# Performance work log

Hardware: AMD Instinct MI355X
Metric: run time of the kernel (lower is better)

Reference implementation:

```python
import jax, jax.numpy as jnp
import numpy as np

EMB = 768
HEADS = 8
HEAD_DIM = EMB // HEADS  # 96


def setup_inputs() -> dict:
    key = jax.random.key(0)
    ks = jax.random.split(key, 9)
    B, S = 16, 1024
    s = 1.0 / np.sqrt(EMB)
    inp = {
        "input_embeddings": jax.random.normal(ks[0], (B, S, EMB), dtype=jnp.float32),
        "Wq": jax.random.normal(ks[1], (EMB, EMB), dtype=jnp.float32) * s,
        "bq": jnp.zeros((EMB,), dtype=jnp.float32),
        "Wk": jax.random.normal(ks[2], (EMB, EMB), dtype=jnp.float32) * s,
        "bk": jnp.zeros((EMB,), dtype=jnp.float32),
        "Wv": jax.random.normal(ks[3], (EMB, EMB), dtype=jnp.float32) * s,
        "bv": jnp.zeros((EMB,), dtype=jnp.float32),
        "Wo": jax.random.normal(ks[4], (EMB, EMB), dtype=jnp.float32) * s,
        "bo": jnp.zeros((EMB,), dtype=jnp.float32),
    }
    return inp


def reference(input_embeddings, Wq, bq, Wk, bk, Wv, bv, Wo, bo):
    B, S, _ = input_embeddings.shape
    # QKV projections (torch Linear: x @ W.T + b; here W stored as [in,out])
    q = input_embeddings @ Wq + bq
    k = input_embeddings @ Wk + bk
    v = input_embeddings @ Wv + bv
    # [B, H, S, Dh]
    q = q.reshape(B, S, HEADS, HEAD_DIM).transpose(0, 2, 1, 3)
    k = k.reshape(B, S, HEADS, HEAD_DIM).transpose(0, 2, 1, 3)
    v = v.reshape(B, S, HEADS, HEAD_DIM).transpose(0, 2, 1, 3)
    scores = jnp.einsum("bhqd,bhkd->bhqk", q, k) / np.sqrt(HEAD_DIM)
    probs = jax.nn.softmax(scores, axis=-1)  # dropout=0 (eval)
    context = jnp.einsum("bhqk,bhkd->bhqd", probs, v)
    context = context.transpose(0, 2, 1, 3).reshape(B, S, HEADS * HEAD_DIM)
    output = context @ Wo + bo
    return (output, probs)
```

## Files before the change

kernel.cpp:

```cpp
#include <hip/hip_runtime.h>

typedef _Float16 half8 __attribute__((ext_vector_type(8)));
typedef _Float16 half4 __attribute__((ext_vector_type(4)));
typedef float f32x4 __attribute__((ext_vector_type(4)));

__device__ __forceinline__ void lds_load16(const void* g, void* l) {
  __builtin_amdgcn_global_load_lds((const __attribute__((address_space(1))) void*)g,
                                   (__attribute__((address_space(3))) void*)l, 16, 0, 0);
}

__global__ __launch_bounds__(256) void cvt_all(const float* __restrict__ X,
                                               const float* __restrict__ Wq, const float* __restrict__ Wk,
                                               const float* __restrict__ Wv, const float* __restrict__ Wo,
                                               _Float16* __restrict__ Xh,
                                               _Float16* __restrict__ Wqkvt, _Float16* __restrict__ Wot) {
  const int bid = blockIdx.x, tid = threadIdx.x;
  if (bid < 6144) {
    int i = bid * 256 + tid;
    const float4* p = (const float4*)(X + (size_t)i * 8);
    float4 a = p[0], b = p[1];
    half8 v;
    v[0] = (_Float16)a.x; v[1] = (_Float16)a.y; v[2] = (_Float16)a.z; v[3] = (_Float16)a.w;
    v[4] = (_Float16)b.x; v[5] = (_Float16)b.y; v[6] = (_Float16)b.z; v[7] = (_Float16)b.w;
    *(half8*)(Xh + (size_t)i * 8) = v;
  } else {
    int id = (bid - 6144) * 256 + tid;
    int part = id / 589824;
    int r = id - part * 589824;
    int k = r / 768;
    int n = r - k * 768;
    const float* W = part == 0 ? Wq : part == 1 ? Wk : part == 2 ? Wv : Wo;
    _Float16 v = (_Float16)W[(size_t)k * 768 + n];
    if (part < 3) Wqkvt[((size_t)(part * 768 + n)) * 768 + k] = v;
    else          Wot[(size_t)n * 768 + k] = v;
  }
}

template <int EPI, int NB>
__global__ __launch_bounds__(256, 4) void gemm128(
    const _Float16* __restrict__ A, const _Float16* __restrict__ Bt,
    const float* __restrict__ b0, const float* __restrict__ b1, const float* __restrict__ b2,
    _Float16* __restrict__ Qo, _Float16* __restrict__ Ko, _Float16* __restrict__ Vto,
    float* __restrict__ Co) {
  __shared__ _Float16 Ab[2][128 * 32];
  __shared__ _Float16 Bb[2][128 * 32];
  const int tid = threadIdx.x, w = tid >> 6, l = tid & 63;
  const int lr = l & 15, lk = l >> 4;
  const int wm = w >> 1, wn = w & 1;
  const int q8 = (int)gridDim.x >> 3;
  const int wg = ((int)blockIdx.x & 7) * q8 + ((int)blockIdx.x >> 3);
  const int m0 = (wg / NB) * 128, n0 = (wg % NB) * 128;

  auto STAGE = [&](int kt, int dstb) {
#pragma unroll
    for (int i = 0; i < 2; ++i) {
      const int g = i * 256 + tid;
      const int row = g >> 2;
      const int gr = (g & 3) ^ (row & 3);
      lds_load16(A + (size_t)(m0 + row) * 768 + kt * 32 + gr * 8,
                 (char*)&Ab[dstb][0] + g * 16);
      lds_load16(Bt + (size_t)(n0 + row) * 768 + kt * 32 + gr * 8,
                 (char*)&Bb[dstb][0] + g * 16);
    }
  };

  f32x4 acc[4][4] = {};
  STAGE(0, 0);
  const int swzg = ((lk ^ (lr & 3)) * 8);

  for (int T = 0; T < 24; ++T) {
    const int b = T & 1;
    asm volatile("s_waitcnt vmcnt(0)" ::: "memory");
    asm volatile("s_barrier" ::: "memory");
    if (T < 23) STAGE(T + 1, b ^ 1);
    half8 af[4], bf[4];
#pragma unroll
    for (int mi = 0; mi < 4; ++mi)
      af[mi] = *(const half8*)&Ab[b][(wm * 64 + mi * 16 + lr) * 32 + swzg];
#pragma unroll
    for (int ni = 0; ni < 4; ++ni)
      bf[ni] = *(const half8*)&Bb[b][(wn * 64 + ni * 16 + lr) * 32 + swzg];
    __builtin_amdgcn_s_setprio(1);
#pragma unroll
    for (int mi = 0; mi < 4; ++mi)
#pragma unroll
      for (int ni = 0; ni < 4; ++ni)
        acc[mi][ni] = __builtin_amdgcn_mfma_f32_16x16x32_f16(af[mi], bf[ni], acc[mi][ni], 0, 0, 0);
    __builtin_amdgcn_s_setprio(0);
  }

#pragma unroll
  for (int mi = 0; mi < 4; ++mi) {
    const int rbase = m0 + wm * 64 + mi * 16 + lk * 4;
#pragma unroll
    for (int ni = 0; ni < 4; ++ni) {
      const int col = n0 + wn * 64 + ni * 16 + lr;
      if (EPI == 0) {
        const int part = col / 768;
        const int e = col - part * 768;
        const int h = e / 96, d = e - (e / 96) * 96;
        const float* bb = part == 0 ? b0 : part == 1 ? b1 : b2;
        const float bv = bb[e];
#pragma unroll
        for (int j = 0; j < 4; ++j) {
          const int row = rbase + j;
          const int bI = row >> 10, s = row & 1023;
          const int bh = bI * 8 + h;
          const _Float16 v = (_Float16)(acc[mi][ni][j] + bv);
          if (part < 2) {
            const size_t idx = ((((size_t)(bh * 64 + (s >> 4)) * 3 + (d >> 5)) * 64
                                + ((d & 31) >> 3) * 16 + (s & 15)) << 3) + (d & 7);
            if (part == 0) Qo[idx] = v; else Ko[idx] = v;
          } else {
            const size_t idx = ((((size_t)(bh * 6 + (d >> 4)) * 32 + (s >> 5)) * 64
                                + ((s & 31) >> 3) * 16 + (d & 15)) << 3) + (s & 7);
            Vto[idx] = v;
          }
        }
      } else {
        const float bv = b0[col];
#pragma unroll
        for (int j = 0; j < 4; ++j) {
          const int row = rbase + j;
          __builtin_nontemporal_store(acc[mi][ni][j] + bv, Co + (size_t)row * 768 + col);
        }
      }
    }
  }
}

__global__ __launch_bounds__(512, 4) void attn(const _Float16* __restrict__ swzQ,
                                               const _Float16* __restrict__ swzK,
                                               const _Float16* __restrict__ swzV,
                                               float* __restrict__ probs,
                                               _Float16* __restrict__ ctx) {
  __shared__ _Float16 Ps[8][2][16][136];
  __shared__ float lsb[8][2][16];
  const int tid = threadIdx.x, w = tid >> 6, l = tid & 63;
  const int lr = l & 15, lk = l >> 4;
  const int id = blockIdx.x;
  const int lid = (id & 7) * 512 + (id >> 3);
  const int bh = lid >> 5, qt2 = lid & 31;
  const int q0 = qt2 * 32;
  const float SC = 0.10206207261596577f * 1.4426950408889634f;
  const int b = bh >> 3, h = bh & 7;

  const half8* qbA = (const half8*)swzQ + (size_t)(bh * 64 + qt2 * 2) * 192;
  const half8* kb  = (const half8*)swzK + (size_t)(bh * 64 + w * 8) * 192;
  const half8* vb0 = (const half8*)swzV + (size_t)bh * 12288;

  half8 bqA[3], bqB[3];
#pragma unroll
  for (int kk = 0; kk < 3; ++kk) { bqA[kk] = qbA[kk * 64 + l]; bqB[kk] = qbA[192 + kk * 64 + l]; }

  f32x4 sA[8], sB[8];
#pragma unroll
  for (int cb = 0; cb < 4; ++cb) {
    half8 kf[2][3];
#pragma unroll
    for (int t = 0; t < 2; ++t)
#pragma unroll
      for (int kk = 0; kk < 3; ++kk) kf[t][kk] = kb[((cb * 2 + t) * 3 + kk) * 64 + l];
#pragma unroll
    for (int t = 0; t < 2; ++t) {
      const int ct = cb * 2 + t;
      f32x4 aA = {0.f, 0.f, 0.f, 0.f}, aB = {0.f, 0.f, 0.f, 0.f};
#pragma unroll
      for (int kk = 0; kk < 3; ++kk) {
        aA = __builtin_amdgcn_mfma_f32_16x16x32_f16(kf[t][kk], bqA[kk], aA, 0, 0, 0);
        aB = __builtin_amdgcn_mfma_f32_16x16x32_f16(kf[t][kk], bqB[kk], aB, 0, 0, 0);
      }
      sA[ct] = aA; sB[ct] = aB;
    }
  }

  float psA = 0.f, psB = 0.f;
#pragma unroll
  for (int ct = 0; ct < 8; ++ct)
#pragma unroll
    for (int j = 0; j < 4; ++j) {
      const float eA = __builtin_amdgcn_exp2f(sA[ct][j] * SC);
      const float eB = __builtin_amdgcn_exp2f(sB[ct][j] * SC);
      sA[ct][j] = eA; psA += eA;
      sB[ct][j] = eB; psB += eB;
    }
  psA += __shfl_xor(psA, 16); psA += __shfl_xor(psA, 32);
  psB += __shfl_xor(psB, 16); psB += __shfl_xor(psB, 32);
  if (lk == 0) { lsb[w][0][lr] = psA; lsb[w][1][lr] = psB; }
  __syncthreads();
  float ltA = 0.f, ltB = 0.f;
#pragma unroll
  for (int ww = 0; ww < 8; ++ww) { ltA += lsb[ww][0][lr]; ltB += lsb[ww][1][lr]; }
  const float invlA = 1.f / ltA, invlB = 1.f / ltB;

  float* pbA = probs + ((size_t)bh << 20) + (size_t)(q0 + lr) * 1024 + w * 128 + lk * 4;
#pragma unroll
  for (int ct = 0; ct < 8; ++ct) {
    f32x4 pA4, pB4;
    half4 phA, phB;
#pragma unroll
    for (int j = 0; j < 4; ++j) {
      const float pA = sA[ct][j] * invlA;
      const float pB = sB[ct][j] * invlB;
      pA4[j] = pA; phA[j] = (_Float16)pA;
      pB4[j] = pB; phB[j] = (_Float16)pB;
    }
    __builtin_nontemporal_store(pA4, (f32x4*)(pbA + ct * 16));
    __builtin_nontemporal_store(pB4, (f32x4*)(pbA + 16 * 1024 + ct * 16));
    *(half4*)&Ps[w][0][lr][ct * 16 + lk * 4] = phA;
    *(half4*)&Ps[w][1][lr][ct * 16 + lk * 4] = phB;
  }

  f32x4 cA[6] = {}, cB[6] = {};
#pragma unroll
  for (int kk = 0; kk < 4; ++kk) {
    half8 vf[6];
#pragma unroll
    for (int dt = 0; dt < 6; ++dt) vf[dt] = vb0[(dt * 32 + w * 4 + kk) * 64 + l];
    half8 paA = *(const half8*)&Ps[w][0][lr][kk * 32 + lk * 8];
    half8 paB = *(const half8*)&Ps[w][1][lr][kk * 32 + lk * 8];
#pragma unroll
    for (int dt = 0; dt < 6; ++dt) {
      cA[dt] = __builtin_amdgcn_mfma_f32_16x16x32_f16(paA, vf[dt], cA[dt], 0, 0, 0);
      cB[dt] = __builtin_amdgcn_mfma_f32_16x16x32_f16(paB, vf[dt], cB[dt], 0, 0, 0);
    }
  }

  _Float16* cpA = &Ps[w][0][0][0];
  _Float16* cpB = &Ps[w][1][0][0];
#pragma unroll
  for (int dt = 0; dt < 6; ++dt)
#pragma unroll
    for (int j = 0; j < 4; ++j) {
      cpA[(lk * 4 + j) * 100 + dt * 16 + lr] = (_Float16)cA[dt][j];
      cpB[(lk * 4 + j) * 100 + dt * 16 + lr] = (_Float16)cB[dt][j];
    }
  __syncthreads();

  const int rq = tid >> 5;
  const int rd0 = (tid & 31) * 3;
#pragma unroll
  for (int t = 0; t < 2; ++t) {
    _Float16* cg = ctx + ((size_t)(b * 1024 + q0 + t * 16 + rq)) * 768 + h * 96 + rd0;
#pragma unroll
    for (int e = 0; e < 3; ++e) {
      float v = 0.f;
#pragma unroll
      for (int ww = 0; ww < 8; ++ww)
        v += (float)((const _Float16*)&Ps[ww][t][0][0])[rq * 100 + rd0 + e];
      cg[e] = (_Float16)v;
    }
  }
}

extern "C" void kernel_launch(void* const* d_in, const int* in_sizes, int n_in,
                              void* d_out, int out_size, void* d_ws, size_t ws_size,
                              hipStream_t stream) {
  (void)in_sizes; (void)n_in; (void)out_size; (void)ws_size;
  const float* X  = (const float*)d_in[0];
  const float* Wq = (const float*)d_in[1];
  const float* bq = (const float*)d_in[2];
  const float* Wk = (const float*)d_in[3];
  const float* bk = (const float*)d_in[4];
  const float* Wv = (const float*)d_in[5];
  const float* bv = (const float*)d_in[6];
  const float* Wo = (const float*)d_in[7];
  const float* bo = (const float*)d_in[8];

  char* ws = (char*)d_ws;
  _Float16* Xh    = (_Float16*)(ws + 0);
  _Float16* Wqkvt = (_Float16*)(ws + 25165824);
  _Float16* Wot   = (_Float16*)(ws + 28704768);
  _Float16* Qh    = (_Float16*)(ws + 29884416);
  _Float16* Kh    = (_Float16*)(ws + 55050240);
  _Float16* Vth   = (_Float16*)(ws + 80216064);
  _Float16* Ctx   = (_Float16*)(ws + 105381888);

  float* out   = (float*)d_out;
  float* probs = out + 12582912;

  cvt_all<<<dim3(15360), dim3(256), 0, stream>>>(X, Wq, Wk, Wv, Wo, Xh, Wqkvt, Wot);
  gemm128<0, 18><<<dim3(2304), dim3(256), 0, stream>>>(Xh, Wqkvt, bq, bk, bv, Qh, Kh, Vth, nullptr);
  attn<<<dim3(4096), dim3(512), 0, stream>>>(Qh, Kh, Vth, probs, Ctx);
  gemm128<1, 6><<<dim3(768), dim3(256), 0, stream>>>(Ctx, Wot, bo, bo, bo, nullptr, nullptr, nullptr, out);
}
```

Measured before the change: 371.8 us.

## Tile weight transpose through LDS and defer softmax normalization in attention

The weight conversion now transposes 64x64 tiles through shared memory with coalesced float4 reads and half4 writes, replacing the per-element strided scatter, and the grid shrinks to match. In attention, unnormalized exp values are written as fp16 straight into LDS, dropping the 32 f32x4 score registers. Probs are then re-read from LDS, scaled by a per-row inverse, and stored with a coalesced row layout. The P·V result is scaled by the inverse sum afterwards, and some barriers become raw s_waitcnt/s_barrier. This lowers register pressure and uncoalesced traffic, but the stored probs now pass through fp16 before normalization, which costs some precision.

```diff
diff --git a/kernel.cpp b/kernel.cpp
--- a/kernel.cpp
+++ b/kernel.cpp
@@ -7,6 +7,11 @@
 __device__ __forceinline__ void lds_load16(const void* g, void* l) {
   __builtin_amdgcn_global_load_lds((const __attribute__((address_space(1))) void*)g,
                                    (__attribute__((address_space(3))) void*)l, 16, 0, 0);
+}
+
+__device__ __forceinline__ void lds_barrier() {
+  asm volatile("s_waitcnt lgkmcnt(0)" ::: "memory");
+  asm volatile("s_barrier" ::: "memory");
 }
 
 __global__ __launch_bounds__(256) void cvt_all(const float* __restrict__ X,
@@ -24,15 +29,32 @@
     v[4] = (_Float16)b.x; v[5] = (_Float16)b.y; v[6] = (_Float16)b.z; v[7] = (_Float16)b.w;
     *(half8*)(Xh + (size_t)i * 8) = v;
   } else {
-    int id = (bid - 6144) * 256 + tid;
-    int part = id / 589824;
-    int r = id - part * 589824;
-    int k = r / 768;
-    int n = r - k * 768;
+    __shared__ _Float16 T[64][72];
+    const int t = bid - 6144;
+    const int part = t / 144;
+    const int r = t - part * 144;
+    const int k0 = (r / 12) * 64, n0 = (r - (r / 12) * 12) * 64;
     const float* W = part == 0 ? Wq : part == 1 ? Wk : part == 2 ? Wv : Wo;
-    _Float16 v = (_Float16)W[(size_t)k * 768 + n];
-    if (part < 3) Wqkvt[((size_t)(part * 768 + n)) * 768 + k] = v;
-    else          Wot[(size_t)n * 768 + k] = v;
+    const int lr0 = tid >> 4, lc0 = (tid & 15) * 4;
+#pragma unroll
+    for (int rr = 0; rr < 4; ++rr) {
+      const int row = lr0 + rr * 16;
+      float4 v = *(const float4*)(W + (size_t)(k0 + row) * 768 + n0 + lc0);
+      T[lc0 + 0][row] = (_Float16)v.x;
+      T[lc0 + 1][row] = (_Float16)v.y;
+      T[lc0 + 2][row] = (_Float16)v.z;
+      T[lc0 + 3][row] = (_Float16)v.w;
+    }
+    __syncthreads();
+    _Float16* Wt = part < 3 ? (Wqkvt + (size_t)(part * 768 + n0) * 768 + k0)
+                            : (Wot + (size_t)n0 * 768 + k0);
+    const int wr0 = tid >> 4, wc0 = (tid & 15) * 4;
+#pragma unroll
+    for (int rr = 0; rr < 4; ++rr) {
+      const int nrow = wr0 + rr * 16;
+      half4 h = *(const half4*)&T[nrow][wc0];
+      *(half4*)(Wt + (size_t)nrow * 768 + wc0) = h;
+    }
   }
 }
 
@@ -134,8 +156,9 @@
                                                const _Float16* __restrict__ swzV,
                                                float* __restrict__ probs,
                                                _Float16* __restrict__ ctx) {
-  __shared__ _Float16 Ps[8][2][16][136];
+  __shared__ __align__(16) _Float16 Ph[8][2][16][136];
   __shared__ float lsb[8][2][16];
+  __shared__ float invb[2][16];
   const int tid = threadIdx.x, w = tid >> 6, l = tid & 63;
   const int lr = l & 15, lk = l >> 4;
   const int id = blockIdx.x;
@@ -153,14 +176,15 @@
 #pragma unroll
   for (int kk = 0; kk < 3; ++kk) { bqA[kk] = qbA[kk * 64 + l]; bqB[kk] = qbA[192 + kk * 64 + l]; }
 
-  f32x4 sA[8], sB[8];
+  float psA = 0.f, psB = 0.f;
 #pragma unroll
   for (int cb = 0; cb < 4; ++cb) {
     half8 kf[2][3];
 #pragma unroll
     for (int t = 0; t < 2; ++t)
 #pragma unroll
-      for (int kk = 0; kk < 3; ++kk) kf[t][kk] = kb[((cb * 2 + t) * 3 + kk) * 64 + l];
+      for (int kk = 0; kk < 3; ++kk)
+        kf[t][kk] = kb[((cb * 2 + t) * 3 + kk) * 64 + l];
 #pragma unroll
     for (int t = 0; t < 2; ++t) {
       const int ct = cb * 2 + t;
@@ -170,46 +194,54 @@
         aA = __builtin_amdgcn_mfma_f32_16x16x32_f16(kf[t][kk], bqA[kk], aA, 0, 0, 0);
         aB = __builtin_amdgcn_mfma_f32_16x16x32_f16(kf[t][kk], bqB[kk], aB, 0, 0, 0);
       }
-      sA[ct] = aA; sB[ct] = aB;
-    }
-  }
-
-  float psA = 0.f, psB = 0.f;
-#pragma unroll
-  for (int ct = 0; ct < 8; ++ct)
-#pragma unroll
-    for (int j = 0; j < 4; ++j) {
-      const float eA = __builtin_amdgcn_exp2f(sA[ct][j] * SC);
-      const float eB = __builtin_amdgcn_exp2f(sB[ct][j] * SC);
-      sA[ct][j] = eA; psA += eA;
-      sB[ct][j] = eB; psB += eB;
-    }
+      half4 hA, hB;
+#pragma unroll
+      for (int j = 0; j < 4; ++j) {
+        const float eA = __builtin_amdgcn_exp2f(aA[j] * SC);
+        const float eB = __builtin_amdgcn_exp2f(aB[j] * SC);
+        psA += eA; psB += eB;
+        hA[j] = (_Float16)eA; hB[j] = (_Float16)eB;
+      }
+      *(half4*)&Ph[w][0][lr][ct * 16 + lk * 4] = hA;
+      *(half4*)&Ph[w][1][lr][ct * 16 + lk * 4] = hB;
+    }
+  }
   psA += __shfl_xor(psA, 16); psA += __shfl_xor(psA, 32);
   psB += __shfl_xor(psB, 16); psB += __shfl_xor(psB, 32);
   if (lk == 0) { lsb[w][0][lr] = psA; lsb[w][1][lr] = psB; }
-  __syncthreads();
-  float ltA = 0.f, ltB = 0.f;
-#pragma unroll
-  for (int ww = 0; ww < 8; ++ww) { ltA += lsb[ww][0][lr]; ltB += lsb[ww][1][lr]; }
-  const float invlA = 1.f / ltA, invlB = 1.f / ltB;
-
-  float* pbA = probs + ((size_t)bh << 20) + (size_t)(q0 + lr) * 1024 + w * 128 + lk * 4;
-#pragma unroll
-  for (int ct = 0; ct < 8; ++ct) {
-    f32x4 pA4, pB4;
-    half4 phA, phB;
-#pragma unroll
-    for (int j = 0; j < 4; ++j) {
-      const float pA = sA[ct][j] * invlA;
-      const float pB = sB[ct][j] * invlB;
-      pA4[j] = pA; phA[j] = (_Float16)pA;
-      pB4[j] = pB; phB[j] = (_Float16)pB;
-    }
-    __builtin_nontemporal_store(pA4, (f32x4*)(pbA + ct * 16));
-    __builtin_nontemporal_store(pB4, (f32x4*)(pbA + 16 * 1024 + ct * 16));
-    *(half4*)&Ps[w][0][lr][ct * 16 + lk * 4] = phA;
-    *(half4*)&Ps[w][1][lr][ct * 16 + lk * 4] = phB;
-  }
+  lds_barrier();
+  if (tid < 32) {
+    const int t = tid >> 4, q = tid & 15;
+    float lt = 0.f;
+#pragma unroll
+    for (int ww = 0; ww < 8; ++ww) lt += lsb[ww][t][q];
+    invb[t][q] = 1.f / lt;
+  }
+  lds_barrier();
+
+  {
+    const int qh = l >> 5, c4 = (l & 31) * 4;
+#pragma unroll
+    for (int t = 0; t < 2; ++t) {
+      float* pbase = probs + ((size_t)bh << 20) + (size_t)(q0 + t * 16) * 1024 + w * 128;
+#pragma unroll
+      for (int r2 = 0; r2 < 8; ++r2) {
+        const int q = r2 * 2 + qh;
+        half4 hv = *(const half4*)&Ph[w][t][q][c4];
+        const float iv = invb[t][q];
+        f32x4 v;
+#pragma unroll
+        for (int j = 0; j < 4; ++j) v[j] = (float)hv[j] * iv;
+        __builtin_nontemporal_store(v, (f32x4*)(pbase + (size_t)q * 1024 + c4));
+      }
+    }
+  }
+
+  float ivr[2][4];
+#pragma unroll
+  for (int t = 0; t < 2; ++t)
+#pragma unroll
+    for (int j = 0; j < 4; ++j) ivr[t][j] = invb[t][lk * 4 + j];
 
   f32x4 cA[6] = {}, cB[6] = {};
 #pragma unroll
@@ -217,8 +249,8 @@
     half8 vf[6];
 #pragma unroll
     for (int dt = 0; dt < 6; ++dt) vf[dt] = vb0[(dt * 32 + w * 4 + kk) * 64 + l];
-    half8 paA = *(const half8*)&Ps[w][0][lr][kk * 32 + lk * 8];
-    half8 paB = *(const half8*)&Ps[w][1][lr][kk * 32 + lk * 8];
+    half8 paA = *(const half8*)&Ph[w][0][lr][kk * 32 + lk * 8];
+    half8 paB = *(const half8*)&Ph[w][1][lr][kk * 32 + lk * 8];
 #pragma unroll
     for (int dt = 0; dt < 6; ++dt) {
       cA[dt] = __builtin_amdgcn_mfma_f32_16x16x32_f16(paA, vf[dt], cA[dt], 0, 0, 0);
@@ -226,16 +258,16 @@
     }
   }
 
-  _Float16* cpA = &Ps[w][0][0][0];
-  _Float16* cpB = &Ps[w][1][0][0];
+  _Float16* cpA = &Ph[w][0][0][0];
+  _Float16* cpB = &Ph[w][1][0][0];
 #pragma unroll
   for (int dt = 0; dt < 6; ++dt)
 #pragma unroll
     for (int j = 0; j < 4; ++j) {
-      cpA[(lk * 4 + j) * 100 + dt * 16 + lr] = (_Float16)cA[dt][j];
-      cpB[(lk * 4 + j) * 100 + dt * 16 + lr] = (_Float16)cB[dt][j];
-    }
-  __syncthreads();
+      cpA[(lk * 4 + j) * 100 + dt * 16 + lr] = (_Float16)(cA[dt][j] * ivr[0][j]);
+      cpB[(lk * 4 + j) * 100 + dt * 16 + lr] = (_Float16)(cB[dt][j] * ivr[1][j]);
+    }
+  lds_barrier();
 
   const int rq = tid >> 5;
   const int rd0 = (tid & 31) * 3;
@@ -247,7 +279,7 @@
       float v = 0.f;
 #pragma unroll
       for (int ww = 0; ww < 8; ++ww)
-        v += (float)((const _Float16*)&Ps[ww][t][0][0])[rq * 100 + rd0 + e];
+        v += (float)((const _Float16*)&Ph[ww][t][0][0])[rq * 100 + rd0 + e];
       cg[e] = (_Float16)v;
     }
   }
@@ -279,7 +311,7 @@
   float* out   = (float*)d_out;
   float* probs = out + 12582912;
 
-  cvt_all<<<dim3(15360), dim3(256), 0, stream>>>(X, Wq, Wk, Wv, Wo, Xh, Wqkvt, Wot);
+  cvt_all<<<dim3(6720), dim3(256), 0, stream>>>(X, Wq, Wk, Wv, Wo, Xh, Wqkvt, Wot);
   gemm128<0, 18><<<dim3(2304), dim3(256), 0, stream>>>(Xh, Wqkvt, bq, bk, bv, Qh, Kh, Vth, nullptr);
   attn<<<dim3(4096), dim3(512), 0, stream>>>(Qh, Kh, Vth, probs, Ctx);
   gemm128<1, 6><<<dim3(768), dim3(256), 0, stream>>>(Ctx, Wot, bo, bo, bo, nullptr, nullptr, nullptr, out);
```

Measured after the change: 340.1 us. -8.5%, faster.
